# Performance work log

Hardware: AMD Instinct MI355X
Metric: run time of the kernel (lower is better)

The kernel has to match this reference:

```python
import jax, jax.numpy as jnp
import numpy as np

B, S, D = 4, 2048, 1024
H, DK, DV = 16, 64, 64
SCALE = 8.0  # scaling_factor = sqrt(dk)


def setup_inputs() -> dict:
    key = jax.random.key(0)
    ks = jax.random.split(key, 9)
    s = 1.0 / np.sqrt(D)
    return {
        "q": jax.random.normal(ks[0], (B, S, D), jnp.float32),
        "k": jax.random.normal(ks[1], (B, S, D), jnp.float32),
        "v": jax.random.normal(ks[2], (B, S, D), jnp.float32),
        "Wq": jax.random.uniform(ks[3], (D, H * DK), jnp.float32, -s, s),
        "bq": jax.random.uniform(ks[4], (H * DK,), jnp.float32, -s, s),
        "Wk": jax.random.uniform(ks[5], (D, H * DK), jnp.float32, -s, s),
        "bk": jax.random.uniform(ks[6], (H * DK,), jnp.float32, -s, s),
        "Wv": jax.random.uniform(ks[7], (D, H * DV), jnp.float32, -s, s),
        "bv": jax.random.uniform(ks[8], (H * DV,), jnp.float32, -s, s),
    }


def reference(q, k, v, Wq, bq, Wk, bk, Wv, bv):
    # Linear projections, then split heads: [B,S,H*d] -> [B,S,H,d]
    qh = (q @ Wq + bq).reshape(B, S, H, DK)
    kh = (k @ Wk + bk).reshape(B, S, H, DK)
    vh = (v @ Wv + bv).reshape(B, S, H, DV)
    # scores: [B,H,Sq,Sk]
    e = jnp.einsum("bqhd,bkhd->bhqk", qh, kh) / SCALE
    attn = jax.nn.softmax(e, axis=-1)
    out = jnp.einsum("bhqk,bkhd->bqhd", attn, vh)  # [B,Sq,H,DV]
    return out.reshape(B, S, H * DV)  # dropout p=0 -> identity
```

## Files before the change

kernel.cpp:

```cpp
#include <hip/hip_runtime.h>
#include <hip/hip_bf16.h>


typedef unsigned short u16;
typedef unsigned int   u32;
typedef short bf16x8 __attribute__((ext_vector_type(8)));
typedef short bf16x4 __attribute__((ext_vector_type(4)));
typedef float f32x4  __attribute__((ext_vector_type(4)));
typedef u32   u32x4  __attribute__((ext_vector_type(4)));

#define S_TOT 2048
#define HD    1024
#define QK_SCALE 0.18033688f

#if __has_builtin(__builtin_amdgcn_exp2f)
#define EXP2(x) __builtin_amdgcn_exp2f(x)
#else
#define EXP2(x) exp2f(x)
#endif

__device__ __forceinline__ u16 f2bf(float f) {
  union { float f; unsigned u; } v; v.f = f;
  unsigned r = v.u + 0x7FFFu + ((v.u >> 16) & 1u);
  return (u16)(r >> 16);
}

__device__ __forceinline__ u32 cvt_pk_bf16(float lo, float hi) {
  u32 r;
  asm("v_cvt_pk_bf16_f32 %0, %1, %2" : "=v"(r) : "v"(lo), "v"(hi));
  return r;
}

__device__ __forceinline__ bf16x4 ds_tr16(unsigned a) {
  bf16x4 d;
  asm volatile("ds_read_b64_tr_b16 %0, %1" : "=v"(d) : "v"(a) : "memory");
  return d;
}

__device__ __forceinline__ void gld16(const u16* g, u16* l) {
  __builtin_amdgcn_global_load_lds(
      (const __attribute__((address_space(1))) u32*)g,
      (__attribute__((address_space(3))) u32*)l, 16, 0, 0);
}

#define LGKM_FENCE() do { asm volatile("s_waitcnt lgkmcnt(0)" ::: "memory"); \
                          __builtin_amdgcn_sched_barrier(0); } while (0)

#define PIPE_BAR(N) do { asm volatile("s_waitcnt vmcnt(" #N ")" ::: "memory"); \
                         __builtin_amdgcn_s_barrier(); \
                         __builtin_amdgcn_sched_barrier(0); } while (0)

__global__ __launch_bounds__(256)
void conv_kernel(const float* __restrict__ x0, const float* __restrict__ x1, const float* __restrict__ x2,
                 const float* __restrict__ w0, const float* __restrict__ w1, const float* __restrict__ w2,
                 u16* __restrict__ Xb, u16* __restrict__ Wt)
{
  const int z = blockIdx.y;
  const int t = threadIdx.x;
  if (blockIdx.x < 1024) {
    const float* X = z == 0 ? x0 : (z == 1 ? x1 : x2);
    u16* Xz = Xb + (size_t)z * 8388608;
    int tid = blockIdx.x * 256 + t;
#pragma unroll
    for (int i = 0; i < 8; ++i) {
      int c = tid + i * 262144;
      int row = c >> 8, k4 = (c & 255) * 4;
      const float4 xv = *(const float4*)&X[(size_t)row * 1024 + k4];
      int p = (k4 & ~31) + 8 * ((k4 & 15) >> 2) + 4 * ((k4 >> 4) & 1);
      p ^= (row & 6) << 2;
      bf16x4 sv = { (short)f2bf(xv.x), (short)f2bf(xv.y), (short)f2bf(xv.z), (short)f2bf(xv.w) };
      *(bf16x4*)&Xz[(size_t)row * 1024 + p] = sv;
    }
  } else {
    const float* W = z == 0 ? w0 : (z == 1 ? w1 : w2);
    u16* Wz = Wt + (size_t)z * 1048576;
    int tid = (blockIdx.x - 1024) * 256 + t;
#pragma unroll
    for (int i = 0; i < 8; ++i) {
      int c = tid + i * 32768;
      int n = c & 1023, k4 = (c >> 10) * 4;
      float wv0 = W[(size_t)(k4 + 0) * 1024 + n];
      float wv1 = W[(size_t)(k4 + 1) * 1024 + n];
      float wv2 = W[(size_t)(k4 + 2) * 1024 + n];
      float wv3 = W[(size_t)(k4 + 3) * 1024 + n];
      int kl = k4 & 31;
      int kp = 8 * ((kl & 15) >> 2) + 4 * ((kl >> 4) & 1);
      int off = ((n >> 7) * 32 + (k4 >> 5)) * 4096 + (n & 127) * 32 + kp;
      bf16x4 sv = { (short)f2bf(wv0), (short)f2bf(wv1), (short)f2bf(wv2), (short)f2bf(wv3) };
      *(bf16x4*)&Wz[off] = sv;
    }
  }
}

__global__ __launch_bounds__(512)
void gemm_kernel(const u16* __restrict__ Xb, const u16* __restrict__ Wt,
                 const float* __restrict__ b0, const float* __restrict__ b1, const float* __restrict__ b2,
                 u16* __restrict__ o0, u16* __restrict__ o1, u16* __restrict__ vT)
{
  int p  = blockIdx.x + 8 * blockIdx.y + 256 * blockIdx.z;
  int wk = (p & 7) * 96 + (p >> 3);
  int nb = wk & 7, mb = (wk >> 3) & 31, z = wk >> 8;

  const u16* Xz = Xb + (size_t)z * 8388608;
  const u16* Wz = Wt + (size_t)z * 1048576;
  const float* BS = z == 0 ? b0 : (z == 1 ? b1 : b2);
  const float  osc = (z == 0) ? QK_SCALE : 1.0f;

  const int t = threadIdx.x;
  const int lane = t & 63, wid = t >> 6;
  const int g = lane >> 4, ln = lane & 15;
  const int wm = wid >> 1;
  const int whalf = wid & 1;
  const int mbase = mb * 256, nbase = nb * 128;
  const int xr = (ln & 6) << 2;

  __shared__ __align__(16) u16 Al[4][256 * 32];

  f32x4 acc[4][4];
#pragma unroll
  for (int i = 0; i < 4; ++i)
#pragma unroll
    for (int j = 0; j < 4; ++j) { acc[i][j][0]=0.f; acc[i][j][1]=0.f; acc[i][j][2]=0.f; acc[i][j][3]=0.f; }

  const u16* sa = Xz + (size_t)(mbase + (t >> 2)) * 1024 + (t & 3) * 8;
  u16* alw[4] = { &Al[0][wid * 512], &Al[1][wid * 512], &Al[2][wid * 512], &Al[3][wid * 512] };

  auto stage = [&](int kb, int buf) __attribute__((always_inline)) {
    gld16(sa + kb * 32,                alw[buf]);
    gld16(sa + kb * 32 + 128 * 1024,   alw[buf] + 4096);
  };

  const u16* wfp = Wz + (size_t)(nb * 32) * 4096 + (whalf * 64 + ln) * 32 + g * 8;
  auto loadB = [&](int kb, bf16x8* dst) __attribute__((always_inline)) {
#pragma unroll
    for (int nf = 0; nf < 4; ++nf)
      dst[nf] = *(const bf16x8*)(wfp + (size_t)kb * 4096 + nf * 512);
  };

  bf16x8 bA[4], bB[4];

  stage(0, 0);
  stage(1, 1);
  loadB(0, bA);
  PIPE_BAR(4);

  if (z < 2) {
    u16* O = z == 0 ? o0 : o1;

    auto compute = [&](int cur, const bf16x8* bq) __attribute__((always_inline)) {
      bf16x8 af[4];
#pragma unroll
      for (int mf = 0; mf < 4; ++mf)
        af[mf] = *(const bf16x8*)&Al[cur][(wm * 64 + mf * 16 + ln) * 32 + (g * 8 ^ xr)];
      __builtin_amdgcn_s_setprio(1);
#pragma unroll
      for (int mf = 0; mf < 4; ++mf)
#pragma unroll
        for (int nf = 0; nf < 4; ++nf)
          acc[mf][nf] = __builtin_amdgcn_mfma_f32_16x16x32_bf16(af[mf], bq[nf], acc[mf][nf], 0, 0, 0);
      __builtin_amdgcn_s_setprio(0);
    };

    for (int j = 0; j < 14; j += 2) {
      int kb = 2 * j;
      stage(kb + 2, 2); stage(kb + 3, 3); loadB(kb + 1, bB); compute(0, bA);
      loadB(kb + 2, bA); compute(1, bB); PIPE_BAR(4);
      stage(kb + 4, 0); stage(kb + 5, 1); loadB(kb + 3, bB); compute(2, bA);
      loadB(kb + 4, bA); compute(3, bB); PIPE_BAR(4);
    }
    stage(30, 2); stage(31, 3); loadB(29, bB); compute(0, bA);
    loadB(30, bA); compute(1, bB); PIPE_BAR(4);
    loadB(31, bB); compute(2, bA); compute(3, bB);

#pragma unroll
    for (int nf = 0; nf < 4; ++nf) {
      int n = nbase + whalf * 64 + nf * 16 + ln;
      float bv = BS[n];
#pragma unroll
      for (int mf = 0; mf < 4; ++mf)
#pragma unroll
        for (int r = 0; r < 4; ++r) {
          int m = mbase + wm * 64 + mf * 16 + 4 * g + r;
          O[(size_t)m * 1024 + n] = f2bf((acc[mf][nf][r] + bv) * osc);
        }
    }
  } else {
    auto compute2 = [&](int cur, const bf16x8* wq) __attribute__((always_inline)) {
      bf16x8 bfx[4];
#pragma unroll
      for (int nf = 0; nf < 4; ++nf)
        bfx[nf] = *(const bf16x8*)&Al[cur][(wm * 64 + nf * 16 + ln) * 32 + (g * 8 ^ xr)];
      __builtin_amdgcn_s_setprio(1);
#pragma unroll
      for (int mf = 0; mf < 4; ++mf)
#pragma unroll
        for (int nf = 0; nf < 4; ++nf)
          acc[mf][nf] = __builtin_amdgcn_mfma_f32_16x16x32_bf16(wq[mf], bfx[nf], acc[mf][nf], 0, 0, 0);
      __builtin_amdgcn_s_setprio(0);
    };

    for (int j = 0; j < 14; j += 2) {
      int kb = 2 * j;
      stage(kb + 2, 2); stage(kb + 3, 3); loadB(kb + 1, bB); compute2(0, bA);
      loadB(kb + 2, bA); compute2(1, bB); PIPE_BAR(4);
      stage(kb + 4, 0); stage(kb + 5, 1); loadB(kb + 3, bB); compute2(2, bA);
      loadB(kb + 4, bA); compute2(3, bB); PIPE_BAR(4);
    }
    stage(30, 2); stage(31, 3); loadB(29, bB); compute2(0, bA);
    loadB(30, bA); compute2(1, bB); PIPE_BAR(4);
    loadB(31, bB); compute2(2, bA); compute2(3, bB);

#pragma unroll
    for (int mf = 0; mf < 4; ++mf)
#pragma unroll
      for (int r = 0; r < 4; ++r) {
        int dvg = nbase + whalf * 64 + mf * 16 + 4 * g + r;
        float bv = BS[dvg];
        int hh = dvg >> 6, dvl = dvg & 63;
#pragma unroll
        for (int nf = 0; nf < 4; ++nf) {
          int m = mbase + wm * 64 + nf * 16 + ln;
          int bb = m >> 11, ss = m & 2047;
          vT[((size_t)(bb * 16 + hh) * 64 + dvl) * 2048 + ss] = f2bf(acc[mf][nf][r] + bv);
        }
      }
  }
}

__global__ __launch_bounds__(256)
void proj_kernel(const float* __restrict__ x0, const float* __restrict__ x1, const float* __restrict__ x2,
                 const float* __restrict__ w0, const float* __restrict__ w1, const float* __restrict__ w2,
                 const float* __restrict__ b0, const float* __restrict__ b1, const float* __restrict__ b2,
                 u16* __restrict__ o0, u16* __restrict__ o1, u16* __restrict__ vT)
{
  int p  = blockIdx.x + 8 * blockIdx.y + 512 * blockIdx.z;
  int wk = (p & 7) * 192 + (p >> 3);
  int nb = wk & 7, mb = (wk >> 3) & 63, z = wk >> 9;

  const float* X  = z == 0 ? x0 : (z == 1 ? x1 : x2);
  const float* W  = z == 0 ? w0 : (z == 1 ? w1 : w2);
  const float* BS = z == 0 ? b0 : (z == 1 ? b1 : b2);
  const float  osc = (z == 0) ? QK_SCALE : 1.0f;

  const int t = threadIdx.x;
  const int lane = t & 63, wid = t >> 6;
  const int g = lane >> 4, ln = lane & 15;
  const int wm = wid >> 1, wn = wid & 1;
  const int mbase = mb * 128, nbase = nb * 128;

  __shared__ __align__(16) u16 As[128 * 40];
  __shared__ __align__(16) u16 Bs[16 * 272];

  f32x4 acc[4][4];
#pragma unroll
  for (int i = 0; i < 4; ++i)
#pragma unroll
    for (int j = 0; j < 4; ++j) { acc[i][j][0]=0.f; acc[i][j][1]=0.f; acc[i][j][2]=0.f; acc[i][j][3]=0.f; }

  const int arow = t >> 3;
  const int ak0  = (t & 7) * 4;
  const int ap   = 8 * ((ak0 & 15) >> 2) + 4 * (ak0 >> 4);
  const int bkr  = t >> 5;
  const int bnc  = (t & 31) * 4;
  const int bnblk = bnc >> 4, bncl = bnc & 15;

  const unsigned bs_base = (unsigned)(size_t)&Bs[0];

  for (int kb = 0; kb < 32; ++kb) {
    const int kbase = kb * 32;
#pragma unroll
    for (int ps = 0; ps < 4; ++ps) {
      int row = arow + 32 * ps;
      const float4 xv = *(const float4*)&X[(size_t)(mbase + row) * 1024 + kbase + ak0];
      bf16x4 sv = { (short)f2bf(xv.x), (short)f2bf(xv.y), (short)f2bf(xv.z), (short)f2bf(xv.w) };
      *(bf16x4*)&As[row * 40 + ap] = sv;
    }
#pragma unroll
    for (int ps = 0; ps < 4; ++ps) {
      int kr = bkr + 8 * ps;
      const float4 wv = *(const float4*)&W[(size_t)(kbase + kr) * 1024 + nbase + bnc];
      bf16x4 sv = { (short)f2bf(wv.x), (short)f2bf(wv.y), (short)f2bf(wv.z), (short)f2bf(wv.w) };
      *(bf16x4*)&Bs[(bnblk * 2 + (kr >> 4)) * 272 + (kr & 15) * 16 + bncl] = sv;
    }
    __syncthreads();

    bf16x8 af[4];
#pragma unroll
    for (int mf = 0; mf < 4; ++mf)
      af[mf] = *(const bf16x8*)&As[(wm * 64 + mf * 16 + ln) * 40 + g * 8];

    bf16x8 bfv[4];
#pragma unroll
    for (int nf = 0; nf < 4; ++nf) {
      unsigned base = bs_base + (unsigned)(((wn * 4 + nf) * 2) * 544) + lane * 8;
      bf16x4 lo = ds_tr16(base);
      bf16x4 hi = ds_tr16(base + 544);
      bf16x8 bb;
      bb[0]=lo[0]; bb[1]=lo[1]; bb[2]=lo[2]; bb[3]=lo[3];
      bb[4]=hi[0]; bb[5]=hi[1]; bb[6]=hi[2]; bb[7]=hi[3];
      bfv[nf] = bb;
    }
    LGKM_FENCE();
#pragma unroll
    for (int mf = 0; mf < 4; ++mf)
#pragma unroll
      for (int nf = 0; nf < 4; ++nf)
        acc[mf][nf] = __builtin_amdgcn_mfma_f32_16x16x32_bf16(af[mf], bfv[nf], acc[mf][nf], 0, 0, 0);
    __syncthreads();
  }

#pragma unroll
  for (int nf = 0; nf < 4; ++nf) {
    int n = nbase + wn * 64 + nf * 16 + ln;
    float bv = BS[n];
#pragma unroll
    for (int mf = 0; mf < 4; ++mf)
#pragma unroll
      for (int r = 0; r < 4; ++r) {
        int m = mbase + wm * 64 + mf * 16 + 4 * g + r;
        float val = (acc[mf][nf][r] + bv) * osc;
        if (z < 2) {
          u16* O = z == 0 ? o0 : o1;
          O[(size_t)m * 1024 + n] = f2bf(val);
        } else {
          vT[((size_t)((m >> 11) * 16 + (n >> 6)) * 64 + (n & 63)) * 2048 + (m & 2047)] = f2bf(val);
        }
      }
  }
}

__global__ __launch_bounds__(512)
void attn_kernel(const u16* __restrict__ qh, const u16* __restrict__ kh, const u16* __restrict__ vT,
                 float* __restrict__ out)
{
  int p  = blockIdx.x + 8 * blockIdx.y + 128 * blockIdx.z;
  int wk = (p & 7) * 64 + (p >> 3);
  int qt = wk & 7, h = (wk >> 3) & 15, b = wk >> 7;

  const int t = threadIdx.x;
  const int lane = t & 63, wid = t >> 6;
  const int g = lane >> 4, ln = lane & 15;
  const size_t bS = (size_t)b * S_TOT;
  const int qwin = qt * 256 + wid * 32;

  __shared__ __align__(16) u16 Ks[64 * 72];
  __shared__ __align__(16) u16 Vt[64 * 72];

  bf16x8 qf[2][2];
#pragma unroll
  for (int nf = 0; nf < 2; ++nf) {
    const u16* qrow = &qh[(bS + qwin + nf * 16 + ln) * HD + h * 64];
#pragma unroll
    for (int kk = 0; kk < 2; ++kk) {
      bf16x4 lo = *(const bf16x4*)&qrow[kk * 32 + 4 * g];
      bf16x4 hi = *(const bf16x4*)&qrow[kk * 32 + 4 * g + 16];
      bf16x8 qq;
      qq[0]=lo[0]; qq[1]=lo[1]; qq[2]=lo[2]; qq[3]=lo[3];
      qq[4]=hi[0]; qq[5]=hi[1]; qq[6]=hi[2]; qq[7]=hi[3];
      qf[nf][kk] = qq;
    }
  }

  bf16x8 ones;
#pragma unroll
  for (int j = 0; j < 8; ++j) ones[j] = (short)0x3F80;

  f32x4 o[2][4];
#pragma unroll
  for (int i = 0; i < 2; ++i)
#pragma unroll
    for (int j = 0; j < 4; ++j) { o[i][j][0]=0.f; o[i][j][1]=0.f; o[i][j][2]=0.f; o[i][j][3]=0.f; }
  f32x4 o1[2];
  o1[0][0]=0.f; o1[0][1]=0.f; o1[0][2]=0.f; o1[0][3]=0.f;
  o1[1][0]=0.f; o1[1][1]=0.f; o1[1][2]=0.f; o1[1][3]=0.f;

  const int skv = t >> 4;
  const int sd0 = (t & 15) * 4;
  const int kpos = 32 * (sd0 >> 5) + 8 * ((sd0 & 15) >> 2) + 4 * ((sd0 >> 4) & 1);
  u16* ksw[2];
  ksw[0] = &Ks[skv * 72 + kpos];
  ksw[1] = &Ks[(skv + 32) * 72 + kpos];
  const u16* kp = &kh[(bS + skv) * HD + h * 64 + sd0];

  const int vdv  = t >> 3;
  const int vkv8 = (t & 7) * 8;
  const int vp0  = 32 * (vkv8 >> 5) + 8 * ((vkv8 & 15) >> 2) + 4 * ((vkv8 >> 4) & 1);
  const int vkv4 = vkv8 + 4;
  const int vp1  = 32 * (vkv4 >> 5) + 8 * ((vkv4 & 15) >> 2) + 4 * ((vkv4 >> 4) & 1);
  u16* vsw0 = &Vt[vdv * 72 + vp0];
  u16* vsw1 = &Vt[vdv * 72 + vp1];
  const u16* vp = &vT[((size_t)(b * 16 + h) * 64 + vdv) * 2048 + vkv8];

  const size_t KSTEP = (size_t)64 * HD, C32 = (size_t)32 * HD;

  bf16x4 kr[2];
  kr[0] = *(const bf16x4*)kp; kr[1] = *(const bf16x4*)(kp + C32);
  bf16x8 vr = *(const bf16x8*)vp;
  kp += KSTEP; vp += 64;

  for (int it = 0; it < 32; ++it) {
    *(bf16x4*)ksw[0] = kr[0];
    *(bf16x4*)ksw[1] = kr[1];
    bf16x4 vlo = { vr[0], vr[1], vr[2], vr[3] };
    bf16x4 vhi = { vr[4], vr[5], vr[6], vr[7] };
    *(bf16x4*)vsw0 = vlo;
    *(bf16x4*)vsw1 = vhi;
    __syncthreads();

    if (it < 31) {
      kr[0] = *(const bf16x4*)kp; kr[1] = *(const bf16x4*)(kp + C32);
      vr = *(const bf16x8*)vp;
      kp += KSTEP; vp += 64;
    }

#pragma unroll
    for (int s = 0; s < 2; ++s) {
      bf16x8 kf[2][2];
#pragma unroll
      for (int mf = 0; mf < 2; ++mf)
#pragma unroll
        for (int kk = 0; kk < 2; ++kk)
          kf[mf][kk] = *(const bf16x8*)&Ks[(s * 32 + mf * 16 + ln) * 72 + kk * 32 + 8 * g];

      f32x4 sc[2][2];
      __builtin_amdgcn_s_setprio(1);
#pragma unroll
      for (int mf = 0; mf < 2; ++mf)
#pragma unroll
        for (int nf = 0; nf < 2; ++nf) {
          f32x4 a; a[0]=0.f; a[1]=0.f; a[2]=0.f; a[3]=0.f;
#pragma unroll
          for (int kk = 0; kk < 2; ++kk)
            a = __builtin_amdgcn_mfma_f32_16x16x32_bf16(kf[mf][kk], qf[nf][kk], a, 0, 0, 0);
          sc[mf][nf] = a;
        }
      __builtin_amdgcn_s_setprio(0);

      bf16x8 vf[4];
#pragma unroll
      for (int nf = 0; nf < 4; ++nf)
        vf[nf] = *(const bf16x8*)&Vt[(nf * 16 + ln) * 72 + s * 32 + 8 * g];

      bf16x8 pa[2];
#pragma unroll
      for (int nf = 0; nf < 2; ++nf) {
        float pv[2][4];
#pragma unroll
        for (int mf = 0; mf < 2; ++mf)
#pragma unroll
          for (int r = 0; r < 4; ++r)
            pv[mf][r] = EXP2(sc[mf][nf][r]);
        union { u32x4 u; bf16x8 b; } pk;
        pk.u[0] = cvt_pk_bf16(pv[0][0], pv[0][1]);
        pk.u[1] = cvt_pk_bf16(pv[0][2], pv[0][3]);
        pk.u[2] = cvt_pk_bf16(pv[1][0], pv[1][1]);
        pk.u[3] = cvt_pk_bf16(pv[1][2], pv[1][3]);
        pa[nf] = pk.b;
      }

      __builtin_amdgcn_s_setprio(1);
#pragma unroll
      for (int mq = 0; mq < 2; ++mq) {
#pragma unroll
        for (int nf = 0; nf < 4; ++nf)
          o[mq][nf] = __builtin_amdgcn_mfma_f32_16x16x32_bf16(pa[mq], vf[nf], o[mq][nf], 0, 0, 0);
        o1[mq] = __builtin_amdgcn_mfma_f32_16x16x32_bf16(pa[mq], ones, o1[mq], 0, 0, 0);
      }
      __builtin_amdgcn_s_setprio(0);
    }
    __syncthreads();
  }

#pragma unroll
  for (int mq = 0; mq < 2; ++mq)
#pragma unroll
    for (int r = 0; r < 4; ++r) {
      float inv = 1.0f / o1[mq][r];
      int qrow = qwin + mq * 16 + 4 * g + r;
#pragma unroll
      for (int nf = 0; nf < 4; ++nf)
        out[(bS + qrow) * HD + h * 64 + nf * 16 + ln] = o[mq][nf][r] * inv;
    }
}

extern "C" void kernel_launch(void* const* d_in, const int* in_sizes, int n_in,
                              void* d_out, int out_size, void* d_ws, size_t ws_size,
                              hipStream_t stream) {
  const float* q  = (const float*)d_in[0];
  const float* k  = (const float*)d_in[1];
  const float* v  = (const float*)d_in[2];
  const float* Wq = (const float*)d_in[3];
  const float* bq = (const float*)d_in[4];
  const float* Wk = (const float*)d_in[5];
  const float* bk = (const float*)d_in[6];
  const float* Wv = (const float*)d_in[7];
  const float* bv = (const float*)d_in[8];
  float* out = (float*)d_out;

  u16* qh = (u16*)d_ws;
  u16* kh = qh + (size_t)8192 * 1024;
  u16* vT = kh + (size_t)8192 * 1024;

  const size_t XB_OFF = (size_t)3 * 8192 * 1024;
  const size_t WT_OFF = XB_OFF + (size_t)3 * 8192 * 1024;
  const size_t NEED   = (WT_OFF + (size_t)3 * 1024 * 1024) * 2;

  if (ws_size >= NEED) {
    u16* Xb = (u16*)d_ws + XB_OFF;
    u16* Wt = (u16*)d_ws + WT_OFF;
    conv_kernel<<<dim3(1152, 3), 256, 0, stream>>>(q, k, v, Wq, Wk, Wv, Xb, Wt);
    gemm_kernel<<<dim3(8, 32, 3), 512, 0, stream>>>(Xb, Wt, bq, bk, bv, qh, kh, vT);
  } else {
    proj_kernel<<<dim3(8, 64, 3), 256, 0, stream>>>(q, k, v, Wq, Wk, Wv, bq, bk, bv, qh, kh, vT);
  }
  attn_kernel<<<dim3(8, 16, 4), 512, 0, stream>>>(qh, kh, vT, out);
}
```

Before: 183.0 us.

## Stage both GEMM operands through LDS with triple-buffered panelized layout

Both the activation and weight matrices are now written by the conversion kernel into 128-row panel tiles with an XOR-swizzled column layout. The projection GEMM then loads both operands into LDS through a three-stage global_load_lds pipeline, instead of staging only X and reading W fragments directly from global memory. Each k-step is split into two MFMA halves with interleaved prefetch and barriers, and the V path reuses the same loop with the MFMA operands swapped. The aim is better memory-latency hiding and fewer uncoalesced global reads, at the cost of more barriers per iteration.

```diff
diff --git a/kernel.cpp b/kernel.cpp
--- a/kernel.cpp
+++ b/kernel.cpp
@@ -49,6 +49,12 @@
 #define PIPE_BAR(N) do { asm volatile("s_waitcnt vmcnt(" #N ")" ::: "memory"); \
                          __builtin_amdgcn_s_barrier(); \
                          __builtin_amdgcn_sched_barrier(0); } while (0)
+
+__device__ __forceinline__ int pscol(int kl, int rr) {
+  int p0 = 8 * ((kl & 15) >> 2) + 4 * ((kl >> 4) & 1) + (kl & 3);
+  int slot = (p0 >> 3) ^ ((rr >> 1) & 3);
+  return slot * 8 + (p0 & 7);
+}
 
 __global__ __launch_bounds__(256)
 void conv_kernel(const float* __restrict__ x0, const float* __restrict__ x1, const float* __restrict__ x2,
@@ -64,12 +70,12 @@
 #pragma unroll
     for (int i = 0; i < 8; ++i) {
       int c = tid + i * 262144;
-      int row = c >> 8, k4 = (c & 255) * 4;
-      const float4 xv = *(const float4*)&X[(size_t)row * 1024 + k4];
-      int p = (k4 & ~31) + 8 * ((k4 & 15) >> 2) + 4 * ((k4 >> 4) & 1);
-      p ^= (row & 6) << 2;
+      int m = c >> 8, k4 = (c & 255) * 4;
+      const float4 xv = *(const float4*)&X[(size_t)m * 1024 + k4];
+      int panel = m >> 7, rr = m & 127, ks = k4 >> 5;
+      int col = pscol(k4 & 31, rr);
       bf16x4 sv = { (short)f2bf(xv.x), (short)f2bf(xv.y), (short)f2bf(xv.z), (short)f2bf(xv.w) };
-      *(bf16x4*)&Xz[(size_t)row * 1024 + p] = sv;
+      *(bf16x4*)&Xz[(size_t)(panel * 32 + ks) * 4096 + rr * 32 + col] = sv;
     }
   } else {
     const float* W = z == 0 ? w0 : (z == 1 ? w1 : w2);
@@ -83,11 +89,10 @@
       float wv1 = W[(size_t)(k4 + 1) * 1024 + n];
       float wv2 = W[(size_t)(k4 + 2) * 1024 + n];
       float wv3 = W[(size_t)(k4 + 3) * 1024 + n];
-      int kl = k4 & 31;
-      int kp = 8 * ((kl & 15) >> 2) + 4 * ((kl >> 4) & 1);
-      int off = ((n >> 7) * 32 + (k4 >> 5)) * 4096 + (n & 127) * 32 + kp;
+      int panel = n >> 7, rr = n & 127, ks = k4 >> 5;
+      int col = pscol(k4 & 31, rr);
       bf16x4 sv = { (short)f2bf(wv0), (short)f2bf(wv1), (short)f2bf(wv2), (short)f2bf(wv3) };
-      *(bf16x4*)&Wz[off] = sv;
+      *(bf16x4*)&Wz[(size_t)(panel * 32 + ks) * 4096 + rr * 32 + col] = sv;
     }
   }
 }
@@ -97,12 +102,13 @@
                  const float* __restrict__ b0, const float* __restrict__ b1, const float* __restrict__ b2,
                  u16* __restrict__ o0, u16* __restrict__ o1, u16* __restrict__ vT)
 {
-  int p  = blockIdx.x + 8 * blockIdx.y + 256 * blockIdx.z;
+  int p  = blockIdx.x + 8 * blockIdx.y;
   int wk = (p & 7) * 96 + (p >> 3);
-  int nb = wk & 7, mb = (wk >> 3) & 31, z = wk >> 8;
-
-  const u16* Xz = Xb + (size_t)z * 8388608;
-  const u16* Wz = Wt + (size_t)z * 1048576;
+  int z  = wk / 256, r = wk % 256;
+  int mb = r >> 3, nb = r & 7;
+
+  const u16* XzB = Xb + (size_t)z * 8388608;
+  const u16* WzB = Wt + (size_t)z * 1048576;
   const float* BS = z == 0 ? b0 : (z == 1 ? b1 : b2);
   const float  osc = (z == 0) ? QK_SCALE : 1.0f;
 
@@ -110,11 +116,10 @@
   const int lane = t & 63, wid = t >> 6;
   const int g = lane >> 4, ln = lane & 15;
   const int wm = wid >> 1;
-  const int whalf = wid & 1;
+  const int wn = wid & 1;
   const int mbase = mb * 256, nbase = nb * 128;
-  const int xr = (ln & 6) << 2;
-
-  __shared__ __align__(16) u16 Al[4][256 * 32];
+
+  __shared__ __align__(16) u16 Lds[3][3][4096];
 
   f32x4 acc[4][4];
 #pragma unroll
@@ -122,106 +127,109 @@
 #pragma unroll
     for (int j = 0; j < 4; ++j) { acc[i][j][0]=0.f; acc[i][j][1]=0.f; acc[i][j][2]=0.f; acc[i][j][3]=0.f; }
 
-  const u16* sa = Xz + (size_t)(mbase + (t >> 2)) * 1024 + (t & 3) * 8;
-  u16* alw[4] = { &Al[0][wid * 512], &Al[1][wid * 512], &Al[2][wid * 512], &Al[3][wid * 512] };
-
-  auto stage = [&](int kb, int buf) __attribute__((always_inline)) {
-    gld16(sa + kb * 32,                alw[buf]);
-    gld16(sa + kb * 32 + 128 * 1024,   alw[buf] + 4096);
+  auto stageA = [&](int jd, int u, int ks) __attribute__((always_inline)) {
+    const u16* src = XzB + (size_t)((2 * mb + u) * 32 + ks) * 4096 + t * 8;
+    gld16(src, &Lds[jd][u][wid * 512]);
   };
-
-  const u16* wfp = Wz + (size_t)(nb * 32) * 4096 + (whalf * 64 + ln) * 32 + g * 8;
-  auto loadB = [&](int kb, bf16x8* dst) __attribute__((always_inline)) {
+  auto stageB = [&](int jd, int ks) __attribute__((always_inline)) {
+    const u16* src = WzB + (size_t)(nb * 32 + ks) * 4096 + t * 8;
+    gld16(src, &Lds[jd][2][wid * 512]);
+  };
+
+  const int fcol = ((g ^ ((ln >> 1) & 3)) << 3);
+  const int au   = wm >> 1;
+  const int arw  = (wm & 1) * 64;
+
+  const bool swapped = (z == 2);
+
+  stageA(0, 0, 0); stageA(0, 1, 0); stageB(0, 0);
+  stageA(1, 0, 1); stageA(1, 1, 1); stageB(1, 1);
+  PIPE_BAR(3);
+
+  for (int k = 0; k < 32; ++k) {
+    const int j  = k % 3;
+    const int js = (k + 2) % 3;
+    const bool st = (k < 30);
+
+    bf16x8 bw[4], af01[2];
 #pragma unroll
     for (int nf = 0; nf < 4; ++nf)
-      dst[nf] = *(const bf16x8*)(wfp + (size_t)kb * 4096 + nf * 512);
-  };
-
-  bf16x8 bA[4], bB[4];
-
-  stage(0, 0);
-  stage(1, 1);
-  loadB(0, bA);
-  PIPE_BAR(4);
-
-  if (z < 2) {
+      bw[nf] = *(const bf16x8*)&Lds[j][2][(wn * 64 + nf * 16 + ln) * 32 + fcol];
+#pragma unroll
+    for (int mf = 0; mf < 2; ++mf)
+      af01[mf] = *(const bf16x8*)&Lds[j][au][(arw + mf * 16 + ln) * 32 + fcol];
+    if (st) { stageA(js, 0, k + 2); stageA(js, 1, k + 2); }
+    __builtin_amdgcn_s_barrier();
+    __builtin_amdgcn_s_setprio(1);
+    if (!swapped) {
+#pragma unroll
+      for (int mf = 0; mf < 2; ++mf)
+#pragma unroll
+        for (int nf = 0; nf < 4; ++nf)
+          acc[mf][nf] = __builtin_amdgcn_mfma_f32_16x16x32_bf16(af01[mf], bw[nf], acc[mf][nf], 0, 0, 0);
+    } else {
+#pragma unroll
+      for (int mf = 0; mf < 2; ++mf)
+#pragma unroll
+        for (int nf = 0; nf < 4; ++nf)
+          acc[mf][nf] = __builtin_amdgcn_mfma_f32_16x16x32_bf16(bw[nf], af01[mf], acc[mf][nf], 0, 0, 0);
+    }
+    __builtin_amdgcn_s_setprio(0);
+    __builtin_amdgcn_s_barrier();
+
+    bf16x8 af23[2];
+#pragma unroll
+    for (int mf = 0; mf < 2; ++mf)
+      af23[mf] = *(const bf16x8*)&Lds[j][au][(arw + (mf + 2) * 16 + ln) * 32 + fcol];
+    if (st) stageB(js, k + 2);
+    __builtin_amdgcn_s_barrier();
+    __builtin_amdgcn_s_setprio(1);
+    if (!swapped) {
+#pragma unroll
+      for (int mf = 0; mf < 2; ++mf)
+#pragma unroll
+        for (int nf = 0; nf < 4; ++nf)
+          acc[mf + 2][nf] = __builtin_amdgcn_mfma_f32_16x16x32_bf16(af23[mf], bw[nf], acc[mf + 2][nf], 0, 0, 0);
+    } else {
+#pragma unroll
+      for (int mf = 0; mf < 2; ++mf)
+#pragma unroll
+        for (int nf = 0; nf < 4; ++nf)
+          acc[mf + 2][nf] = __builtin_amdgcn_mfma_f32_16x16x32_bf16(bw[nf], af23[mf], acc[mf + 2][nf], 0, 0, 0);
+    }
+    __builtin_amdgcn_s_setprio(0);
+    if (k < 30)      PIPE_BAR(3);
+    else if (k == 30) PIPE_BAR(0);
+    else             __builtin_amdgcn_s_barrier();
+  }
+
+  if (!swapped) {
     u16* O = z == 0 ? o0 : o1;
-
-    auto compute = [&](int cur, const bf16x8* bq) __attribute__((always_inline)) {
-      bf16x8 af[4];
+#pragma unroll
+    for (int nf = 0; nf < 4; ++nf) {
+      int n = nbase + wn * 64 + nf * 16 + ln;
+      float bv = BS[n];
 #pragma unroll
       for (int mf = 0; mf < 4; ++mf)
-        af[mf] = *(const bf16x8*)&Al[cur][(wm * 64 + mf * 16 + ln) * 32 + (g * 8 ^ xr)];
-      __builtin_amdgcn_s_setprio(1);
-#pragma unroll
-      for (int mf = 0; mf < 4; ++mf)
-#pragma unroll
-        for (int nf = 0; nf < 4; ++nf)
-          acc[mf][nf] = __builtin_amdgcn_mfma_f32_16x16x32_bf16(af[mf], bq[nf], acc[mf][nf], 0, 0, 0);
-      __builtin_amdgcn_s_setprio(0);
-    };
-
-    for (int j = 0; j < 14; j += 2) {
-      int kb = 2 * j;
-      stage(kb + 2, 2); stage(kb + 3, 3); loadB(kb + 1, bB); compute(0, bA);
-      loadB(kb + 2, bA); compute(1, bB); PIPE_BAR(4);
-      stage(kb + 4, 0); stage(kb + 5, 1); loadB(kb + 3, bB); compute(2, bA);
-      loadB(kb + 4, bA); compute(3, bB); PIPE_BAR(4);
-    }
-    stage(30, 2); stage(31, 3); loadB(29, bB); compute(0, bA);
-    loadB(30, bA); compute(1, bB); PIPE_BAR(4);
-    loadB(31, bB); compute(2, bA); compute(3, bB);
-
-#pragma unroll
-    for (int nf = 0; nf < 4; ++nf) {
-      int n = nbase + whalf * 64 + nf * 16 + ln;
-      float bv = BS[n];
-#pragma unroll
-      for (int mf = 0; mf < 4; ++mf)
-#pragma unroll
-        for (int r = 0; r < 4; ++r) {
-          int m = mbase + wm * 64 + mf * 16 + 4 * g + r;
-          O[(size_t)m * 1024 + n] = f2bf((acc[mf][nf][r] + bv) * osc);
+#pragma unroll
+        for (int r2 = 0; r2 < 4; ++r2) {
+          int m = mbase + wm * 64 + mf * 16 + 4 * g + r2;
+          O[(size_t)m * 1024 + n] = f2bf((acc[mf][nf][r2] + bv) * osc);
         }
     }
   } else {
-    auto compute2 = [&](int cur, const bf16x8* wq) __attribute__((always_inline)) {
-      bf16x8 bfx[4];
-#pragma unroll
-      for (int nf = 0; nf < 4; ++nf)
-        bfx[nf] = *(const bf16x8*)&Al[cur][(wm * 64 + nf * 16 + ln) * 32 + (g * 8 ^ xr)];
-      __builtin_amdgcn_s_setprio(1);
-#pragma unroll
-      for (int mf = 0; mf < 4; ++mf)
-#pragma unroll
-        for (int nf = 0; nf < 4; ++nf)
-          acc[mf][nf] = __builtin_amdgcn_mfma_f32_16x16x32_bf16(wq[mf], bfx[nf], acc[mf][nf], 0, 0, 0);
-      __builtin_amdgcn_s_setprio(0);
-    };
-
-    for (int j = 0; j < 14; j += 2) {
-      int kb = 2 * j;
-      stage(kb + 2, 2); stage(kb + 3, 3); loadB(kb + 1, bB); compute2(0, bA);
-      loadB(kb + 2, bA); compute2(1, bB); PIPE_BAR(4);
-      stage(kb + 4, 0); stage(kb + 5, 1); loadB(kb + 3, bB); compute2(2, bA);
-      loadB(kb + 4, bA); compute2(3, bB); PIPE_BAR(4);
-    }
-    stage(30, 2); stage(31, 3); loadB(29, bB); compute2(0, bA);
-    loadB(30, bA); compute2(1, bB); PIPE_BAR(4);
-    loadB(31, bB); compute2(2, bA); compute2(3, bB);
-
-#pragma unroll
-    for (int mf = 0; mf < 4; ++mf)
-#pragma unroll
-      for (int r = 0; r < 4; ++r) {
-        int dvg = nbase + whalf * 64 + mf * 16 + 4 * g + r;
+#pragma unroll
+    for (int nf = 0; nf < 4; ++nf)
+#pragma unroll
+      for (int r2 = 0; r2 < 4; ++r2) {
+        int dvg = nbase + wn * 64 + nf * 16 + 4 * g + r2;
         float bv = BS[dvg];
         int hh = dvg >> 6, dvl = dvg & 63;
 #pragma unroll
-        for (int nf = 0; nf < 4; ++nf) {
-          int m = mbase + wm * 64 + nf * 16 + ln;
+        for (int mf = 0; mf < 4; ++mf) {
+          int m = mbase + wm * 64 + mf * 16 + ln;
           int bb = m >> 11, ss = m & 2047;
-          vT[((size_t)(bb * 16 + hh) * 64 + dvl) * 2048 + ss] = f2bf(acc[mf][nf][r] + bv);
+          vT[((size_t)(bb * 16 + hh) * 64 + dvl) * 2048 + ss] = f2bf(acc[mf][nf][r2] + bv);
         }
       }
   }
@@ -509,7 +517,7 @@
     u16* Xb = (u16*)d_ws + XB_OFF;
     u16* Wt = (u16*)d_ws + WT_OFF;
     conv_kernel<<<dim3(1152, 3), 256, 0, stream>>>(q, k, v, Wq, Wk, Wv, Xb, Wt);
-    gemm_kernel<<<dim3(8, 32, 3), 512, 0, stream>>>(Xb, Wt, bq, bk, bv, qh, kh, vT);
+    gemm_kernel<<<dim3(8, 96), 512, 0, stream>>>(Xb, Wt, bq, bk, bv, qh, kh, vT);
   } else {
     proj_kernel<<<dim3(8, 64, 3), 256, 0, stream>>>(q, k, v, Wq, Wk, Wv, bq, bk, bv, qh, kh, vT);
   }
```

New measurement: 180.4 us. No clear change (-1.4%).
